# Kernel optimization log

Measured on AMD Instinct MI355X. Metric: run time of the kernel, lower is better.

## Reference

```python
import jax, jax.numpy as jnp
import numpy as np

B, N, D, H, DH = 64, 512, 128, 4, 32  # graphs, nodes/graph, emb_dim, heads, head_dim
E = 8192  # edges per graph (avg degree 16)


def setup_inputs() -> dict:
    key = jax.random.key(0)
    ks = jax.random.split(key, 12)
    total_nodes = B * N
    # within-graph random edges, then shift to global node ids
    src = jax.random.randint(ks[0], (B, E), 0, N)
    dst = jax.random.randint(ks[1], (B, E), 0, N)
    offs = (jnp.arange(B) * N)[:, None]
    edge_index = jnp.stack([(src + offs).reshape(-1), (dst + offs).reshape(-1)], axis=0)
    batch = jnp.repeat(jnp.arange(B), N)
    inner = H * DH
    s = lambda d: 1.0 / np.sqrt(d)
    return {
        "x": jax.random.normal(ks[2], (total_nodes, D), jnp.float32),
        "edge_index": edge_index,
        "edge_embedding": jax.random.normal(ks[3], (B * E, D), jnp.float32),
        "batch": batch,
        "W_gcn": jax.random.normal(ks[4], (D, D), jnp.float32) * s(D),
        "b_gcn": jnp.zeros((D,), jnp.float32),
        "root_emb": jax.random.normal(ks[5], (1, D), jnp.float32),
        "Wq": jax.random.normal(ks[6], (D, inner), jnp.float32) * s(D),
        "Wkv": jax.random.normal(ks[7], (D, 2 * inner), jnp.float32) * s(D),
        "Wout": jax.random.normal(ks[8], (inner, D), jnp.float32) * s(inner),
        "b_out": jnp.zeros((D,), jnp.float32),
    }


def reference(x, edge_index, edge_embedding, batch, W_gcn, b_gcn, root_emb, Wq, Wkv, Wout, b_out):
    total_nodes = x.shape[0]
    row, col = edge_index[0], edge_index[1]
    # ---- GCNConv ----
    h = x @ W_gcn + b_gcn
    deg = jax.ops.segment_sum(jnp.ones_like(row, dtype=h.dtype), row, num_segments=total_nodes) + 1.0
    dinv = deg ** -0.5  # deg >= 1, no inf
    norm = dinv[row] * dinv[col]
    msg = norm[:, None] * jax.nn.relu(h[row] + edge_embedding)
    agg = jax.ops.segment_sum(msg, col, num_segments=total_nodes)
    h = agg + jax.nn.relu(h + root_emb) / deg[:, None]
    # ---- dense batch (uniform graph sizes -> reshape) + masked self-attention ----
    nf = h.reshape(B, N, D)
    q = (nf @ Wq).reshape(B, N, H, DH)
    kv = nf @ Wkv
    k = kv[..., : H * DH].reshape(B, N, H, DH)
    v = kv[..., H * DH :].reshape(B, N, H, DH)
    scale = DH ** -0.5
    sim = jnp.einsum("bihd,bjhd->bhij", q, k) * scale
    attn = jax.nn.softmax(sim, axis=-1)  # all-true node mask (uniform batches)
    out = jnp.einsum("bhij,bjhd->bihd", attn, v).reshape(B, N, H * DH)
    out = out @ Wout + b_out
    return out.reshape(total_nodes, D)
```

## Files before the change

kernel.cpp:

```cpp
#include <hip/hip_runtime.h>
#include <hip/hip_bf16.h>

#define TOTAL_NODES 32768
#define NNODE 512
#define ETOT 524288

typedef unsigned short u16;
typedef __attribute__((ext_vector_type(8))) short bf16x8;
typedef __attribute__((ext_vector_type(4))) float f32x4;

union U8 { bf16x8 v; u16 s[8]; uint4 q; };

__device__ __forceinline__ float bf2f(u16 u) {
    union { unsigned int i; float f; } x; x.i = ((unsigned int)u) << 16; return x.f;
}
__device__ __forceinline__ u16 f2bf(float f) {
    union { __hip_bfloat16 h; u16 u; } c; c.h = __float2bfloat16(f); return c.u;
}
__device__ __forceinline__ f32x4 mfma16(bf16x8 a, bf16x8 b, f32x4 c) {
    return __builtin_amdgcn_mfma_f32_16x16x32_bf16(a, b, c, 0, 0, 0);
}

__global__ void hist_kernel(const int* __restrict__ ei, int* __restrict__ cnt_row,
                            int* __restrict__ cnt_col) {
    int e = blockIdx.x * blockDim.x + threadIdx.x;
    if (e < ETOT) {
        atomicAdd(&cnt_row[ei[e]], 1);
        atomicAdd(&cnt_col[ei[ETOT + e]], 1);
    }
}

__global__ void dinv_kernel(const int* __restrict__ cnt_row, float* __restrict__ dinv) {
    int n = blockIdx.x * blockDim.x + threadIdx.x;
    if (n < TOTAL_NODES) dinv[n] = rsqrtf((float)cnt_row[n] + 1.0f);
}

__global__ __launch_bounds__(1024) void scan_kernel(const int* __restrict__ cnt,
                                                    int* __restrict__ offs,
                                                    int* __restrict__ cur) {
    __shared__ int part[1024];
    const int t = threadIdx.x;
    const int base = t * 32;
    int local[32];
    int s = 0;
#pragma unroll
    for (int i = 0; i < 32; i++) { local[i] = s; s += cnt[base + i]; }
    part[t] = s;
    __syncthreads();
    for (int off = 1; off < 1024; off <<= 1) {
        int v = (t >= off) ? part[t - off] : 0;
        __syncthreads();
        part[t] += v;
        __syncthreads();
    }
    int prefix = (t == 0) ? 0 : part[t - 1];
#pragma unroll
    for (int i = 0; i < 32; i++) {
        int o = prefix + local[i];
        offs[base + i] = o;
        cur[base + i] = o;
    }
    if (t == 1023) offs[32768] = prefix + s;
}

__global__ void scatter_kernel(const int* __restrict__ ei, int* __restrict__ cur,
                               int2* __restrict__ pairs) {
    int e = blockIdx.x * blockDim.x + threadIdx.x;
    if (e < ETOT) {
        int r = ei[e], c = ei[ETOT + e];
        int pos = atomicAdd(&cur[c], 1);
        pairs[pos] = make_int2(r, e);
    }
}

__global__ __launch_bounds__(128) void gather_kernel(const int2* __restrict__ pairs,
                                                     const int* __restrict__ offs,
                                                     const int* __restrict__ cnt_row,
                                                     const float* __restrict__ dinv,
                                                     const float* __restrict__ h0,
                                                     const float* __restrict__ ee,
                                                     const float* __restrict__ root,
                                                     float* __restrict__ h) {
    const int c = blockIdx.x;
    const int d = threadIdx.x;
    const int s = offs[c], e_end = offs[c + 1];
    float acc = 0.0f;
    int i = s;
    for (; i + 2 <= e_end; i += 2) {
        int2 p0 = pairs[i], p1 = pairs[i + 1];
        float d0 = dinv[p0.x], d1 = dinv[p1.x];
        float v0 = h0[(size_t)p0.x * 128 + d] + ee[(size_t)p0.y * 128 + d];
        float v1 = h0[(size_t)p1.x * 128 + d] + ee[(size_t)p1.y * 128 + d];
        acc += fmaxf(v0, 0.0f) * d0 + fmaxf(v1, 0.0f) * d1;
    }
    for (; i < e_end; i++) {
        int2 p0 = pairs[i];
        float v0 = h0[(size_t)p0.x * 128 + d] + ee[(size_t)p0.y * 128 + d];
        acc += fmaxf(v0, 0.0f) * dinv[p0.x];
    }
    float degc = (float)cnt_row[c] + 1.0f;
    float hv = h0[(size_t)c * 128 + d] + root[d];
    h[(size_t)c * 128 + d] = dinv[c] * acc + fmaxf(hv, 0.0f) / degc;
}

template <int OUTC>
__global__ __launch_bounds__(256) void gemm_kernel(const float* __restrict__ in,
                                                   const float* __restrict__ W,
                                                   const float* __restrict__ bias,
                                                   float* __restrict__ outp) {
    __shared__ __align__(16) float a_lds[8 * 128];
    const int rb = blockIdx.x * 8;
    const int t = threadIdx.x;
    for (int idx = t; idx < 8 * 128; idx += OUTC)
        a_lds[idx] = in[(size_t)(rb + (idx >> 7)) * 128 + (idx & 127)];
    __syncthreads();

    float acc[8];
    float bv = bias ? bias[t] : 0.0f;
#pragma unroll
    for (int r = 0; r < 8; r++) acc[r] = bv;

    const float4* a4 = (const float4*)a_lds;
    for (int k4 = 0; k4 < 32; k4++) {
        float w0 = W[(k4 * 4 + 0) * OUTC + t];
        float w1 = W[(k4 * 4 + 1) * OUTC + t];
        float w2 = W[(k4 * 4 + 2) * OUTC + t];
        float w3 = W[(k4 * 4 + 3) * OUTC + t];
#pragma unroll
        for (int r = 0; r < 8; r++) {
            float4 a = a4[r * 32 + k4];
            acc[r] = fmaf(a.x, w0, fmaf(a.y, w1, fmaf(a.z, w2, fmaf(a.w, w3, acc[r]))));
        }
    }
#pragma unroll
    for (int r = 0; r < 8; r++) outp[(size_t)(rb + r) * OUTC + t] = acc[r];
}

__global__ __launch_bounds__(256) void prep_kernel(const float* __restrict__ kv,
                                                   u16* __restrict__ khi,
                                                   u16* __restrict__ klo,
                                                   u16* __restrict__ vT) {
    __shared__ float vtile[64 * 33];
    const int t = threadIdx.x;
    const int bh = blockIdx.x, b = bh >> 2, h = bh & 3;
    const int hoff = h * 32;
    for (int idx = t; idx < 512 * 32; idx += 256) {
        int n = idx >> 5, d = idx & 31;
        float f = kv[(size_t)(b * 512 + n) * 256 + hoff + d];
        u16 hi = f2bf(f);
        khi[(size_t)bh * 16384 + idx] = hi;
        klo[(size_t)bh * 16384 + idx] = f2bf(f - bf2f(hi));
    }
    for (int c = 0; c < 8; c++) {
        __syncthreads();
        for (int i = t; i < 64 * 32; i += 256) {
            int n0 = i >> 5, d = i & 31;
            vtile[n0 * 33 + d] = kv[(size_t)(b * 512 + c * 64 + n0) * 256 + 128 + hoff + d];
        }
        __syncthreads();
        for (int i = t; i < 32 * 64; i += 256) {
            int d = i >> 6, n0 = i & 63;
            vT[(size_t)(bh * 32 + d) * 512 + c * 64 + n0] = f2bf(vtile[n0 * 33 + d]);
        }
    }
}

__global__ __launch_bounds__(256) void attn_mfma_kernel(const float* __restrict__ qbuf,
                                                        const u16* __restrict__ khi,
                                                        const u16* __restrict__ klo,
                                                        const u16* __restrict__ vT,
                                                        float* __restrict__ ao) {
    __shared__ u16 transit[8][16 * 36];
    const int t = threadIdx.x;
    const int w = t >> 6, L = t & 63;
    const int n16 = L & 15, quad = L >> 4;
    const int bh = blockIdx.y, b = bh >> 2, h = bh & 3;
    const int qbase = blockIdx.x * 128 + w * 32;

    bf16x8 qhi[2], qlo[2];
#pragma unroll
    for (int p = 0; p < 2; p++) {
        const float* qp = qbuf + (size_t)(b * 512 + qbase + p * 16 + n16) * 128 + h * 32 + quad * 8;
        U8 uh, ul;
#pragma unroll
        for (int j = 0; j < 8; j++) {
            float f = qp[j] * 0.17677669529663687f;
            u16 hi = f2bf(f);
            uh.s[j] = hi;
            ul.s[j] = f2bf(f - bf2f(hi));
        }
        qhi[p] = uh.v; qlo[p] = ul.v;
    }

    const f32x4 zero = {0.f, 0.f, 0.f, 0.f};

    float m[2][4];
#pragma unroll
    for (int p = 0; p < 2; p++)
#pragma unroll
        for (int r = 0; r < 4; r++) m[p][r] = -1e30f;

    for (int j0 = 0; j0 < 512; j0 += 16) {
        U8 ub; ub.q = *(const uint4*)(khi + (size_t)(bh * 512 + j0 + n16) * 32 + quad * 8);
#pragma unroll
        for (int p = 0; p < 2; p++) {
            f32x4 s = mfma16(qhi[p], ub.v, zero);
#pragma unroll
            for (int r = 0; r < 4; r++) m[p][r] = fmaxf(m[p][r], s[r]);
        }
    }
#pragma unroll
    for (int p = 0; p < 2; p++)
#pragma unroll
        for (int r = 0; r < 4; r++) {
            float mv = m[p][r];
#pragma unroll
            for (int mask = 1; mask < 16; mask <<= 1) mv = fmaxf(mv, __shfl_xor(mv, mask));
            m[p][r] = mv;
        }

    float l[2][4] = {{0.f, 0.f, 0.f, 0.f}, {0.f, 0.f, 0.f, 0.f}};
    f32x4 O[2][2];
#pragma unroll
    for (int p = 0; p < 2; p++)
#pragma unroll
        for (int dt = 0; dt < 2; dt++) O[p][dt] = zero;

    u16* tr[2] = { transit[w * 2 + 0], transit[w * 2 + 1] };

    for (int jb = 0; jb < 512; jb += 32) {
#pragma unroll
        for (int jt = 0; jt < 2; jt++) {
            const int j0 = jb + jt * 16;
            const size_t kidx = (size_t)(bh * 512 + j0 + n16) * 32 + quad * 8;
            U8 uh; uh.q = *(const uint4*)(khi + kidx);
            U8 ul; ul.q = *(const uint4*)(klo + kidx);
#pragma unroll
            for (int p = 0; p < 2; p++) {
                f32x4 s = mfma16(qhi[p], uh.v, zero);
                s = mfma16(qhi[p], ul.v, s);
                s = mfma16(qlo[p], uh.v, s);
#pragma unroll
                for (int r = 0; r < 4; r++) {
                    float pr = __expf(s[r] - m[p][r]);
                    u16 pb = f2bf(pr);
                    l[p][r] += bf2f(pb);
                    tr[p][(quad * 4 + r) * 36 + jt * 16 + n16] = pb;
                }
            }
        }
        bf16x8 A[2];
#pragma unroll
        for (int p = 0; p < 2; p++) {
            const u16* trp = tr[p];
            const int off = n16 * 36 + quad * 8;
            uint2 lo = *(const uint2*)(trp + off);
            uint2 hi2 = *(const uint2*)(trp + off + 4);
            U8 ua; ua.q = make_uint4(lo.x, lo.y, hi2.x, hi2.y);
            A[p] = ua.v;
        }
#pragma unroll
        for (int dt = 0; dt < 2; dt++) {
            U8 uv; uv.q = *(const uint4*)(vT + (size_t)(bh * 32 + dt * 16 + n16) * 512 + jb + quad * 8);
#pragma unroll
            for (int p = 0; p < 2; p++) O[p][dt] = mfma16(A[p], uv.v, O[p][dt]);
        }
    }

#pragma unroll
    for (int p = 0; p < 2; p++)
#pragma unroll
        for (int r = 0; r < 4; r++) {
            float lv = l[p][r];
#pragma unroll
            for (int mask = 1; mask < 16; mask <<= 1) lv += __shfl_xor(lv, mask);
            float inv = 1.0f / lv;
#pragma unroll
            for (int dt = 0; dt < 2; dt++)
                ao[(size_t)(b * 512 + qbase + p * 16 + quad * 4 + r) * 128 + h * 32 + dt * 16 + n16]
                    = O[p][dt][r] * inv;
        }
}

extern "C" void kernel_launch(void* const* d_in, const int* in_sizes, int n_in,
                              void* d_out, int out_size, void* d_ws, size_t ws_size,
                              hipStream_t stream) {
    const float* x    = (const float*)d_in[0];
    const int*   ei   = (const int*)d_in[1];
    const float* ee   = (const float*)d_in[2];
    const float* Wg   = (const float*)d_in[4];
    const float* bg   = (const float*)d_in[5];
    const float* root = (const float*)d_in[6];
    const float* Wq   = (const float*)d_in[7];
    const float* Wkv  = (const float*)d_in[8];
    const float* Wo   = (const float*)d_in[9];
    const float* bo   = (const float*)d_in[10];

    char* ws = (char*)d_ws;
    int*   cnt_row = (int*)ws;
    float* dinv    = (float*)(ws + 131072);
    float* buf1    = (float*)(ws + 262144);
    float* hbuf    = buf1 + 4194304;
    float* kv      = hbuf + 4194304;
    u16*   khi     = (u16*)hbuf;
    u16*   klo     = khi + 4194304;
    u16*   vT      = (u16*)d_out;
    int*   cnt_col = (int*)kv;
    int*   offs    = cnt_col + 32768;
    int*   cur     = offs + 32769;
    int2*  pairs   = (int2*)(cur + 32768 + 1023);

    hipMemsetAsync(cnt_row, 0, 131072, stream);
    hipMemsetAsync(cnt_col, 0, 131072, stream);

    hist_kernel<<<2048, 256, 0, stream>>>(ei, cnt_row, cnt_col);
    dinv_kernel<<<128, 256, 0, stream>>>(cnt_row, dinv);
    scan_kernel<<<1, 1024, 0, stream>>>(cnt_col, offs, cur);
    scatter_kernel<<<2048, 256, 0, stream>>>(ei, cur, pairs);

    gemm_kernel<128><<<4096, 128, 0, stream>>>(x, Wg, bg, buf1);

    gather_kernel<<<32768, 128, 0, stream>>>(pairs, offs, cnt_row, dinv, buf1, ee, root, hbuf);

    gemm_kernel<128><<<4096, 128, 0, stream>>>(hbuf, Wq, nullptr, buf1);
    gemm_kernel<256><<<4096, 256, 0, stream>>>(hbuf, Wkv, nullptr, kv);

    prep_kernel<<<256, 256, 0, stream>>>(kv, khi, klo, vT);

    attn_mfma_kernel<<<dim3(4, 256), 256, 0, stream>>>(buf1, khi, klo, vT, buf1);

    gemm_kernel<128><<<4096, 128, 0, stream>>>(buf1, Wo, bo, (float*)d_out);
}
```

Baseline: 654.6 us.

## Fuse Q/KV projections with bf16 split and V transpose into one kernel

Merges the Q GEMM, the KV GEMM and the prep kernel into a single qkv_kernel. It reads the activation tile once, writes Q in fp32, writes K as bf16 hi/lo pairs through an LDS staging buffer, and writes V straight into a new blocked transposed layout that the attention kernel now indexes. The dinv computation is also folded into the scan kernel, which drops one launch. This removes the fp32 kv round trip and two launches, at the cost of a wider 384-thread block and a changed vT layout that the attention kernel must match.

```diff
diff --git a/kernel.cpp b/kernel.cpp
--- a/kernel.cpp
+++ b/kernel.cpp
@@ -30,14 +30,11 @@
     }
 }
 
-__global__ void dinv_kernel(const int* __restrict__ cnt_row, float* __restrict__ dinv) {
-    int n = blockIdx.x * blockDim.x + threadIdx.x;
-    if (n < TOTAL_NODES) dinv[n] = rsqrtf((float)cnt_row[n] + 1.0f);
-}
-
 __global__ __launch_bounds__(1024) void scan_kernel(const int* __restrict__ cnt,
                                                     int* __restrict__ offs,
-                                                    int* __restrict__ cur) {
+                                                    int* __restrict__ cur,
+                                                    const int* __restrict__ cnt_row,
+                                                    float* __restrict__ dinv) {
     __shared__ int part[1024];
     const int t = threadIdx.x;
     const int base = t * 32;
@@ -61,6 +58,9 @@
         cur[base + i] = o;
     }
     if (t == 1023) offs[32768] = prefix + s;
+#pragma unroll
+    for (int i = 0; i < 32; i++)
+        dinv[base + i] = rsqrtf((float)cnt_row[base + i] + 1.0f);
 }
 
 __global__ void scatter_kernel(const int* __restrict__ ei, int* __restrict__ cur,
@@ -136,32 +136,74 @@
     for (int r = 0; r < 8; r++) outp[(size_t)(rb + r) * OUTC + t] = acc[r];
 }
 
-__global__ __launch_bounds__(256) void prep_kernel(const float* __restrict__ kv,
-                                                   u16* __restrict__ khi,
-                                                   u16* __restrict__ klo,
-                                                   u16* __restrict__ vT) {
-    __shared__ float vtile[64 * 33];
+__global__ __launch_bounds__(384) void qkv_kernel(const float* __restrict__ in,
+                                                  const float* __restrict__ Wq,
+                                                  const float* __restrict__ Wkv,
+                                                  float* __restrict__ qout,
+                                                  u16* __restrict__ khi,
+                                                  u16* __restrict__ klo,
+                                                  u16* __restrict__ vT) {
+    __shared__ __align__(16) float a_lds[8 * 128];
+    __shared__ __align__(16) u16 kstage[2][8 * 128];
+    const int rb = blockIdx.x * 8;
     const int t = threadIdx.x;
-    const int bh = blockIdx.x, b = bh >> 2, h = bh & 3;
-    const int hoff = h * 32;
-    for (int idx = t; idx < 512 * 32; idx += 256) {
-        int n = idx >> 5, d = idx & 31;
-        float f = kv[(size_t)(b * 512 + n) * 256 + hoff + d];
-        u16 hi = f2bf(f);
-        khi[(size_t)bh * 16384 + idx] = hi;
-        klo[(size_t)bh * 16384 + idx] = f2bf(f - bf2f(hi));
-    }
-    for (int c = 0; c < 8; c++) {
-        __syncthreads();
-        for (int i = t; i < 64 * 32; i += 256) {
-            int n0 = i >> 5, d = i & 31;
-            vtile[n0 * 33 + d] = kv[(size_t)(b * 512 + c * 64 + n0) * 256 + 128 + hoff + d];
-        }
-        __syncthreads();
-        for (int i = t; i < 32 * 64; i += 256) {
-            int d = i >> 6, n0 = i & 63;
-            vT[(size_t)(bh * 32 + d) * 512 + c * 64 + n0] = f2bf(vtile[n0 * 33 + d]);
-        }
+    for (int idx = t; idx < 8 * 128; idx += 384)
+        a_lds[idx] = in[(size_t)(rb + (idx >> 7)) * 128 + (idx & 127)];
+    __syncthreads();
+
+    float acc[8];
+#pragma unroll
+    for (int r = 0; r < 8; r++) acc[r] = 0.0f;
+
+    const float4* a4 = (const float4*)a_lds;
+    const bool isq = (t < 128);
+    const float* Wp = isq ? (Wq + t) : (Wkv + (t - 128));
+    const int ldw = isq ? 128 : 256;
+    for (int k4 = 0; k4 < 32; k4++) {
+        float w0 = Wp[(size_t)(k4 * 4 + 0) * ldw];
+        float w1 = Wp[(size_t)(k4 * 4 + 1) * ldw];
+        float w2 = Wp[(size_t)(k4 * 4 + 2) * ldw];
+        float w3 = Wp[(size_t)(k4 * 4 + 3) * ldw];
+#pragma unroll
+        for (int r = 0; r < 8; r++) {
+            float4 a = a4[r * 32 + k4];
+            acc[r] = fmaf(a.x, w0, fmaf(a.y, w1, fmaf(a.z, w2, fmaf(a.w, w3, acc[r]))));
+        }
+    }
+
+    const int b = rb >> 9;
+    const int rbl = rb & 511;
+
+    if (t < 128) {
+#pragma unroll
+        for (int r = 0; r < 8; r++) qout[(size_t)(rb + r) * 128 + t] = acc[r];
+    } else if (t < 256) {
+        const int c = t - 128;
+#pragma unroll
+        for (int r = 0; r < 8; r++) {
+            u16 hi = f2bf(acc[r]);
+            kstage[0][r * 128 + c] = hi;
+            kstage[1][r * 128 + c] = f2bf(acc[r] - bf2f(hi));
+        }
+    } else {
+        const int c = t - 256;
+        const int h = c >> 5, d = c & 31;
+        const int bh = b * 4 + h;
+        U8 u;
+#pragma unroll
+        for (int r = 0; r < 8; r++) u.s[r] = f2bf(acc[r]);
+        *(uint4*)(vT + ((size_t)(bh * 64 + (rbl >> 3)) * 32 + d) * 8) = u.q;
+    }
+    __syncthreads();
+    if (t < 256) {
+        const int hl = t >> 7;
+        const int u = t & 127;
+        const int h = u >> 5;
+        const int j = u & 31;
+        const int n = j >> 2, dq = j & 3;
+        uint4 val = *(const uint4*)(&kstage[hl][n * 128 + h * 32 + dq * 8]);
+        u16* dst = (hl ? klo : khi) + (size_t)(b * 4 + h) * 16384 + (size_t)(rbl + n) * 32 + dq * 8;
+        *(uint4*)dst = val;
     }
 }
 
@@ -261,7 +303,9 @@
         }
 #pragma unroll
         for (int dt = 0; dt < 2; dt++) {
-            U8 uv; uv.q = *(const uint4*)(vT + (size_t)(bh * 32 + dt * 16 + n16) * 512 + jb + quad * 8);
+            U8 uv; uv.q = *(const uint4*)(vT + (size_t)bh * 16384
+                                          + (size_t)((jb + quad * 8) >> 3) * 256
+                                          + (size_t)(dt * 16 + n16) * 8);
 #pragma unroll
             for (int p = 0; p < 2; p++) O[p][dt] = mfma16(A[p], uv.v, O[p][dt]);
         }
@@ -301,11 +345,11 @@
     float* dinv    = (float*)(ws + 131072);
     float* buf1    = (float*)(ws + 262144);
     float* hbuf    = buf1 + 4194304;
-    float* kv      = hbuf + 4194304;
-    u16*   khi     = (u16*)hbuf;
+    char*  reg3    = (char*)(hbuf + 4194304);
+    u16*   khi     = (u16*)reg3;
     u16*   klo     = khi + 4194304;
     u16*   vT      = (u16*)d_out;
-    int*   cnt_col = (int*)kv;
+    int*   cnt_col = (int*)reg3;
     int*   offs    = cnt_col + 32768;
     int*   cur     = offs + 32769;
     int2*  pairs   = (int2*)(cur + 32768 + 1023);
@@ -314,18 +358,14 @@
     hipMemsetAsync(cnt_col, 0, 131072, stream);
 
     hist_kernel<<<2048, 256, 0, stream>>>(ei, cnt_row, cnt_col);
-    dinv_kernel<<<128, 256, 0, stream>>>(cnt_row, dinv);
-    scan_kernel<<<1, 1024, 0, stream>>>(cnt_col, offs, cur);
+    scan_kernel<<<1, 1024, 0, stream>>>(cnt_col, offs, cur, cnt_row, dinv);
     scatter_kernel<<<2048, 256, 0, stream>>>(ei, cur, pairs);
 
     gemm_kernel<128><<<4096, 128, 0, stream>>>(x, Wg, bg, buf1);
 
     gather_kernel<<<32768, 128, 0, stream>>>(pairs, offs, cnt_row, dinv, buf1, ee, root, hbuf);
 
-    gemm_kernel<128><<<4096, 128, 0, stream>>>(hbuf, Wq, nullptr, buf1);
-    gemm_kernel<256><<<4096, 256, 0, stream>>>(hbuf, Wkv, nullptr, kv);
-
-    prep_kernel<<<256, 256, 0, stream>>>(kv, khi, klo, vT);
+    qkv_kernel<<<4096, 384, 0, stream>>>(hbuf, Wq, Wkv, buf1, khi, klo, vT);
 
     attn_mfma_kernel<<<dim3(4, 256), 256, 0, stream>>>(buf1, khi, klo, vT, buf1);
 
```

Measured after the change: 646.1 us. No clear change (-1.3%).
